# Optimization experiments

Measured on AMD Instinct MI355X. Metric: run time of the kernel, lower is better.

## Reference

```python
import jax, jax.numpy as jnp
import numpy as np

# dims: S slots, B batch, D pred-rep dim, E slot-embedding dim, H hidden/output dim, V per-slot vocab
S, B, D, E, H, V = 7, 4096, 1024, 128, 512, 200
D0 = D + E  # layer-0 LSTM input size


def setup_inputs() -> dict:
    key = jax.random.key(0)
    ks = jax.random.split(key, 12)
    rn = lambda k, shape, s=0.02: jax.random.normal(k, shape, jnp.float32) * s
    return {
        "pred_reps": jax.random.normal(ks[0], (B, D), jnp.float32),
        "slot_labels": jax.random.randint(ks[1], (S, B), 0, V),
        "emb": rn(ks[2], (S, V, E), 1.0),
        # layer 0: per-slot LSTMCell + highway params
        "Wih0": rn(ks[3], (S, 4 * H, D0)), "Whh0": rn(ks[4], (S, 4 * H, H)),
        "bih0": jnp.zeros((S, 4 * H), jnp.float32), "bhh0": jnp.zeros((S, 4 * H), jnp.float32),
        "hwW0": rn(ks[5], (S, H, D0 + H)), "hwb0": jnp.zeros((S, H), jnp.float32),
        "linW0": rn(ks[6], (S, H, D0)),
        # layer 1 (input size = H)
        "Wih1": rn(ks[7], (S, 4 * H, H)), "Whh1": rn(ks[8], (S, 4 * H, H)),
        "bih1": jnp.zeros((S, 4 * H), jnp.float32), "bhh1": jnp.zeros((S, 4 * H), jnp.float32),
        "hwW1": rn(ks[9], (S, H, 2 * H)), "hwb1": jnp.zeros((S, H), jnp.float32),
        "linW1": rn(ks[10], (S, H, H)),
    }


def _lstm_cell(x, h, c, Wih, Whh, bih, bhh):
    # torch LSTMCell: gates ordered i, f, g, o
    gates = x @ Wih.T + bih + h @ Whh.T + bhh
    i, f, g, o = jnp.split(gates, 4, axis=-1)
    c_new = jax.nn.sigmoid(f) * c + jax.nn.sigmoid(i) * jnp.tanh(g)
    h_new = jax.nn.sigmoid(o) * jnp.tanh(c_new)
    return h_new, c_new


def reference(pred_reps, slot_labels, emb, Wih0, Whh0, bih0, bhh0, hwW0, hwb0, linW0,
              Wih1, Whh1, bih1, bhh1, hwW1, hwb1, linW1):
    def step(carry, xs):
        h0, c0, h1, c1 = carry
        (tbl, idx, wih0, whh0, bi0, bh0, hw0, hb0, lw0,
         wih1, whh1, bi1, bh1, hw1, hb1, lw1) = xs
        # per-slot embedding gather + concat with predicate reps  -> [B, D0]
        x = jnp.concatenate([pred_reps, tbl[idx]], axis=-1)
        # layer 0 cell + highway gate
        h0n, c0n = _lstm_cell(x, h0, c0, wih0, whh0, bi0, bh0)
        gate0 = jax.nn.sigmoid(jnp.concatenate([x, h0n], axis=-1) @ hw0.T + hb0)
        x1 = gate0 * h0n + (1.0 - gate0) * (x @ lw0.T)
        # layer 1 cell (its highway output is dead code in the original: curr_input
        # after the last layer is discarded, so we skip it -- same math)
        h1n, c1n = _lstm_cell(x1, h1, c1, wih1, whh1, bi1, bh1)
        return (h0n, c0n, h1n, c1n), None

    init = tuple(jnp.zeros((B, H), pred_reps.dtype) for _ in range(4))
    xs = (emb, slot_labels, Wih0, Whh0, bih0, bhh0, hwW0, hwb0, linW0,
          Wih1, Whh1, bih1, bhh1, hwW1, hwb1, linW1)
    carry, _ = jax.lax.scan(step, init, xs)
    return carry[2]  # last_h: top-layer hidden after final slot
```

## Files before the change

kernel.cpp:

```cpp
#include <hip/hip_runtime.h>
#include <stdint.h>

typedef unsigned short u16;

#define S_   7
#define B_   4096
#define D_   1024
#define E_   128
#define H_   512
#define V_   200
#define D0_  1152
#define XLD  1536
#define K0_  1664
#define KX1  1024
#define G4H  2048

typedef __bf16 bf16x8 __attribute__((ext_vector_type(8)));
typedef float  f32x4  __attribute__((ext_vector_type(4)));
typedef u16    u16x8  __attribute__((ext_vector_type(8)));

__device__ __forceinline__ u16 f2bf(float f) {
  union { float f; uint32_t u; } v; v.f = f;
  uint32_t r = v.u + 0x7fffu + ((v.u >> 16) & 1u);
  return (u16)(r >> 16);
}
__device__ __forceinline__ float bf2f(u16 b) {
  union { uint32_t u; float f; } v; v.u = ((uint32_t)b) << 16;
  return v.f;
}
__device__ __forceinline__ float sigmoidf_(float x) { return 1.0f / (1.0f + __expf(-x)); }
__device__ __forceinline__ float tanhf_(float x) {
  float t = __expf(-2.f * fabsf(x));
  return copysignf((1.f - t) / (1.f + t), x);
}

__device__ __forceinline__ void glds16(const u16* g, u16* l) {
  __builtin_amdgcn_global_load_lds(
      (const __attribute__((address_space(1))) uint32_t*)g,
      (__attribute__((address_space(3))) uint32_t*)l, 16, 0, 0);
}

__device__ __forceinline__ void cvt8(const float* src, u16x8* dst) {
  const float4* p = (const float4*)src;
  float4 x = p[0], y = p[1];
  u16x8 o;
  o[0]=f2bf(x.x); o[1]=f2bf(x.y); o[2]=f2bf(x.z); o[3]=f2bf(x.w);
  o[4]=f2bf(y.x); o[5]=f2bf(y.y); o[6]=f2bf(y.z); o[7]=f2bf(y.w);
  *dst = o;
}

template<int KK, int P1, int P2, int KA, int KB>
__global__ void pack_gw(const float* __restrict__ Wih, const float* __restrict__ Whh,
                        u16* __restrict__ dst) {
  const int CH = KK / 32;
  int i = blockIdx.x * 256 + threadIdx.x;
  int sr = i / CH, c = i - sr * CH;
  int k = c * 32;
  long s = sr >> 11;
  int  r = sr & 2047;
  int  g = r >> 9, j = r & 511;
  long drow = (s << 11) + ((j >> 4) * 64 + g * 16 + (j & 15));
  const float* src = (k < P1) ? Wih + (long)sr * KA + k
                   : (k < P2) ? Whh + (long)sr * KB + (k - P1)
                              : Wih + (long)sr * KA + P1 + (k - P2);
  u16* d = dst + drow * KK + k;
  #pragma unroll
  for (int q = 0; q < 4; ++q) {
    u16x8 o; cvt8(src + q * 8, &o);
    *(u16x8*)(d + q * 8) = o;
  }
}

template<int KS, bool Z2>
__global__ void pack_hw(const float* __restrict__ src, u16* __restrict__ dst, int off16) {
  const int CH = K0_ / 32;
  int i = blockIdx.x * 256 + threadIdx.x;
  int sj = i / CH, c = i - sj * CH;
  int k = c * 32;
  long s = sj >> 9;
  int  j = sj & 511;
  long drow = (s << 10) + ((j >> 4) * 32 + off16 + (j & 15));
  u16* d = dst + drow * K0_ + k;
  if (k >= 1024 && k < 1536 && Z2) {
    u16x8 z = {};
    #pragma unroll
    for (int q = 0; q < 4; ++q) *(u16x8*)(d + q * 8) = z;
    return;
  }
  const float* sp = (k < 1024) ? src + (long)sj * KS + k
                  : (k < 1536) ? src + (long)sj * KS + 1152 + (k - 1024)
                               : src + (long)sj * KS + 1024 + (k - 1536);
  #pragma unroll
  for (int q = 0; q < 4; ++q) {
    u16x8 o; cvt8(sp + q * 8, &o);
    *(u16x8*)(d + q * 8) = o;
  }
}

__global__ void pack_predz(const float* __restrict__ pred, u16* __restrict__ dst) {
  const int CH = XLD / 32;
  int i = blockIdx.x * 256 + threadIdx.x;
  int row = i / CH, c = i - row * CH;
  int k = c * 32;
  u16* d = dst + (long)row * XLD + k;
  if (k < 1024) {
    const float* sp = pred + (long)row * D_ + k;
    #pragma unroll
    for (int q = 0; q < 4; ++q) {
      u16x8 o; cvt8(sp + q * 8, &o);
      *(u16x8*)(d + q * 8) = o;
    }
  } else {
    u16x8 z = {};
    #pragma unroll
    for (int q = 0; q < 4; ++q) *(u16x8*)(d + q * 8) = z;
  }
}

__global__ void xgather(const float* __restrict__ emb, const int* __restrict__ labels,
                        u16* __restrict__ EMB) {
  int b = blockIdx.x;
  int e = threadIdx.x;
  #pragma unroll
  for (int s = 0; s < S_; ++s) {
    int ix = labels[s * B_ + b];
    EMB[((long)(s * B_ + b)) * E_ + e] = f2bf(emb[((long)(s * V_ + ix)) * E_ + e]);
  }
}

__global__ void bias_sum(const float* __restrict__ a, const float* __restrict__ b,
                         float* __restrict__ o, int n) {
  int i = blockIdx.x * 256 + threadIdx.x;
  if (i < n) o[i] = a[i] + b[i];
}
__global__ void zero_f(float* __restrict__ p, int n) {
  for (int i = blockIdx.x * 256 + threadIdx.x; i < n; i += gridDim.x * 256) p[i] = 0.f;
}
__global__ void zero_u16k(u16* __restrict__ p, int n) {
  for (int i = blockIdx.x * 256 + threadIdx.x; i < n; i += gridDim.x * 256) p[i] = 0;
}

template<int MODE>
__global__ __launch_bounds__(256)
void gemm_fused(const u16* __restrict__ A, int lda,
                const u16* __restrict__ EMBs,
                const u16* __restrict__ W, int ldw,
                int K, int TS, int ntn, int cpx,
                const float* __restrict__ bsum,
                float* __restrict__ cbuf,
                u16* __restrict__ hdst, int hld, int hoff,
                float* __restrict__ hf32,
                const u16* __restrict__ xcat0) {
  __shared__ __align__(16) u16 lds[4 * 8192];
  u16* lA = lds;
  u16* lW = lds + 2 * 8192;
  const int tid  = threadIdx.x;
  const int lane = tid & 63;
  const int wave = tid >> 6;
  const int p    = blockIdx.x;
  const int bid  = (p & 7) * cpx + (p >> 3);
  const int tn = bid % ntn;
  const int tm = bid / ntn;
  const long row0 = (long)tm * 128;
  const long col0 = (long)tn * 128;
  const int wm = (wave >> 1) * 64;
  const int wn = (wave & 1) * 64;
  const int fr = lane & 15;
  const int fk = (lane >> 4) * 8;
  const int wr = wave * 32;

  const int srow = wr + (lane >> 3);
  const int scol = ((lane & 7) ^ ((lane >> 3) & 7)) * 8;
  const u16* ga = A + (row0 + srow) * (long)lda + scol;
  const u16* ge = EMBs ? (EMBs + (row0 + srow) * (long)E_ + scol) : nullptr;
  const u16* gw = W + (col0 + srow) * (long)ldw + scol;
  const int dst0 = wr * 64 + lane * 8;

  auto stage = [&](int t, int b) {
    const u16* gb; long ld;
    if (t < TS) { gb = ga + ((long)t << 6);        ld = lda; }
    else        { gb = ge + ((long)(t - TS) << 6); ld = E_;  }
    const u16* gww = gw + ((long)t << 6);
    u16* dA = lA + b * 8192 + dst0;
    u16* dW = lW + b * 8192 + dst0;
    #pragma unroll
    for (int i = 0; i < 4; ++i) {
      glds16(gb  + (long)(i * 8) * ld,  dA + i * 512);
      glds16(gww + (long)(i * 8) * ldw, dW + i * 512);
    }
  };

  int aoff[4], woff[4];
  #pragma unroll
  for (int m = 0; m < 4; ++m) aoff[m] = (wm + m * 16 + fr) * 64;
  #pragma unroll
  for (int n = 0; n < 4; ++n) woff[n] = (wn + n * 16 + fr) * 64;
  const int swz = (fr & 7) << 3;
  const int kk0 = (0 + fk) ^ swz;
  const int kk1 = (32 + fk) ^ swz;

  f32x4 acc[4][4] = {};
  const int nt = K >> 6;

  stage(0, 0);

  for (int t = 0; t < nt; ++t) {
    __syncthreads();
    if (t + 1 < nt) stage(t + 1, (t + 1) & 1);
    const u16* Ab = lA + (t & 1) * 8192;
    const u16* Wb = lW + (t & 1) * 8192;
    bf16x8 af0[4], wf0[4], af1[4], wf1[4];
    #pragma unroll
    for (int m = 0; m < 4; ++m) af0[m] = *(const bf16x8*)&Ab[aoff[m] + kk0];
    #pragma unroll
    for (int n = 0; n < 4; ++n) wf0[n] = *(const bf16x8*)&Wb[woff[n] + kk0];
    #pragma unroll
    for (int m = 0; m < 4; ++m) af1[m] = *(const bf16x8*)&Ab[aoff[m] + kk1];
    #pragma unroll
    for (int n = 0; n < 4; ++n) wf1[n] = *(const bf16x8*)&Wb[woff[n] + kk1];
    #pragma unroll
    for (int m = 0; m < 4; ++m)
      #pragma unroll
      for (int n = 0; n < 4; ++n)
        acc[m][n] = __builtin_amdgcn_mfma_f32_16x16x32_bf16(af0[m], wf0[n], acc[m][n], 0, 0, 0);
    #pragma unroll
    for (int m = 0; m < 4; ++m)
      #pragma unroll
      for (int n = 0; n < 4; ++n)
        acc[m][n] = __builtin_amdgcn_mfma_f32_16x16x32_bf16(af1[m], wf1[n], acc[m][n], 0, 0, 0);
  }

  const int cr = (lane >> 4) * 4;
  const int jg = wn >> 6;

  if (MODE == 0) {
    const int j = tn * 32 + jg * 16 + fr;
    const float bi = bsum[j], bf = bsum[512 + j], bg = bsum[1024 + j], bo = bsum[1536 + j];
    #pragma unroll
    for (int m = 0; m < 4; ++m) {
      const long rbase = row0 + wm + m * 16 + cr;
      #pragma unroll
      for (int r = 0; r < 4; ++r) {
        const long ri = rbase + r;
        float gi = acc[m][0][r] + bi;
        float gf = acc[m][1][r] + bf;
        float gg = acc[m][2][r] + bg;
        float go = acc[m][3][r] + bo;
        float cv = cbuf[ri * H_ + j];
        float cn = sigmoidf_(gf) * cv + sigmoidf_(gi) * tanhf_(gg);
        float hn = sigmoidf_(go) * tanhf_(cn);
        cbuf[ri * H_ + j] = cn;
        hdst[ri * hld + hoff + j] = f2bf(hn);
        if (hf32) hf32[ri * H_ + j] = hn;
      }
    }
  } else {
    #pragma unroll
    for (int pp = 0; pp < 2; ++pp) {
      const int j = tn * 64 + jg * 32 + pp * 16 + fr;
      const float bj = bsum[j];
      #pragma unroll
      for (int m = 0; m < 4; ++m) {
        const long rbase = row0 + wm + m * 16 + cr;
        #pragma unroll
        for (int r = 0; r < 4; ++r) {
          const long ri = rbase + r;
          float gv = sigmoidf_(acc[m][2 * pp][r] + bj);
          float h0 = bf2f(xcat0[ri * XLD + 1024 + j]);
          float x1 = gv * h0 + (1.f - gv) * acc[m][2 * pp + 1][r];
          hdst[ri * hld + hoff + j] = f2bf(x1);
        }
      }
    }
  }
}

extern "C" void kernel_launch(void* const* d_in, const int* in_sizes, int n_in,
                              void* d_out, int out_size, void* d_ws, size_t ws_size,
                              hipStream_t stream) {
  const float* pred   = (const float*)d_in[0];
  const int*   labels = (const int*)d_in[1];
  const float* emb    = (const float*)d_in[2];
  const float* Wih0   = (const float*)d_in[3];
  const float* Whh0   = (const float*)d_in[4];
  const float* bih0   = (const float*)d_in[5];
  const float* bhh0   = (const float*)d_in[6];
  const float* hwW0   = (const float*)d_in[7];
  const float* hwb0   = (const float*)d_in[8];
  const float* linW0  = (const float*)d_in[9];
  const float* Wih1   = (const float*)d_in[10];
  const float* Whh1   = (const float*)d_in[11];
  const float* bih1   = (const float*)d_in[12];
  const float* bhh1   = (const float*)d_in[13];
  float* out = (float*)d_out;

  char* ws = (char*)d_ws;
  size_t off = 0;
  auto alloc = [&](size_t bytes) {
    char* p = ws + off;
    off = (off + bytes + 255) & ~(size_t)255;
    return p;
  };
  u16* WC0   = (u16*)alloc((size_t)S_ * G4H * K0_ * 2);
  u16* WHL   = (u16*)alloc((size_t)S_ * 1024 * K0_ * 2);
  u16* WC1   = (u16*)alloc((size_t)S_ * G4H * KX1 * 2);
  u16* xcat  = (u16*)alloc((size_t)B_ * XLD * 2);
  u16* EMB   = (u16*)alloc((size_t)S_ * B_ * E_ * 2);
  u16* x1cat = (u16*)alloc((size_t)B_ * KX1 * 2);
  float* c0   = (float*)alloc((size_t)B_ * H_ * 4);
  float* c1   = (float*)alloc((size_t)B_ * H_ * 4);
  float* bs0  = (float*)alloc((size_t)S_ * G4H * 4);
  float* bs1  = (float*)alloc((size_t)S_ * G4H * 4);

  pack_gw<K0_, 1024, 1536, D0_, H_><<<2912, 256, 0, stream>>>(Wih0, Whh0, WC0);
  pack_gw<KX1,  512, 1024, H_,  H_><<<1792, 256, 0, stream>>>(Wih1, Whh1, WC1);
  pack_hw<K0_, false><<<728, 256, 0, stream>>>(hwW0,  WHL, 0);
  pack_hw<D0_, true ><<<728, 256, 0, stream>>>(linW0, WHL, 16);
  pack_predz<<<768, 256, 0, stream>>>(pred, xcat);
  xgather<<<B_, E_, 0, stream>>>(emb, labels, EMB);
  bias_sum<<<(S_ * G4H + 255) / 256, 256, 0, stream>>>(bih0, bhh0, bs0, S_ * G4H);
  bias_sum<<<(S_ * G4H + 255) / 256, 256, 0, stream>>>(bih1, bhh1, bs1, S_ * G4H);
  zero_f<<<256, 256, 0, stream>>>(c0, B_ * H_);
  zero_f<<<256, 256, 0, stream>>>(c1, B_ * H_);
  zero_u16k<<<256, 256, 0, stream>>>(x1cat, B_ * KX1);

  const int g0 = (B_ / 128) * (G4H / 128);
  const int g1 = (B_ / 128) * (1024 / 128);

  for (int s = 0; s < S_; ++s) {
    const u16* EMBs = EMB + (size_t)s * B_ * E_;

    gemm_fused<0><<<g0, 256, 0, stream>>>(
        xcat, XLD, EMBs, WC0 + (size_t)s * G4H * K0_, K0_, K0_, 24, G4H / 128, g0 / 8,
        bs0 + (size_t)s * G4H, c0, xcat, XLD, 1024, nullptr, nullptr);

    gemm_fused<1><<<g1, 256, 0, stream>>>(
        xcat, XLD, EMBs, WHL + (size_t)s * 1024 * K0_, K0_, K0_, 24, 1024 / 128, g1 / 8,
        hwb0 + (size_t)s * H_, nullptr, x1cat, KX1, 0, nullptr, xcat);

    gemm_fused<0><<<g0, 256, 0, stream>>>(
        x1cat, KX1, nullptr, WC1 + (size_t)s * G4H * KX1, KX1, KX1, 16, G4H / 128, g0 / 8,
        bs1 + (size_t)s * G4H, c1, x1cat, KX1, H_, out, nullptr);
  }
}
```

Baseline: 699.5 us.

## Wavefront-pipeline the three per-slot GEMMs into one multi-GEMM launch per step

Replaces the 21 sequential per-slot GEMM launches with 9 launches of a combined kernel. Each launch runs layer-0 gates for slot k, the highway step for slot k-1 and layer-1 gates for slot k-2 side by side, using double-buffered (ping-pong) h columns in wider xcat/x1cat buffers to avoid read/write hazards. The goal is fewer launch and tail bubbles and larger grids that keep all CUs busy, at the cost of runtime-dispatched parameters and more workspace. The pack kernels are also rewritten so each thread converts four strided 8-element chunks.

```diff
diff --git a/kernel.cpp b/kernel.cpp
--- a/kernel.cpp
+++ b/kernel.cpp
@@ -10,10 +10,11 @@
 #define H_   512
 #define V_   200
 #define D0_  1152
-#define XLD  1536
 #define K0_  1664
 #define KX1  1024
 #define G4H  2048
+#define XW   2048
+#define X1W  2048
 
 typedef __bf16 bf16x8 __attribute__((ext_vector_type(8)));
 typedef float  f32x4  __attribute__((ext_vector_type(4)));
@@ -40,80 +41,79 @@
       (__attribute__((address_space(3))) uint32_t*)l, 16, 0, 0);
 }
 
-__device__ __forceinline__ void cvt8(const float* src, u16x8* dst) {
+__device__ __forceinline__ void cvt8s(const float* src, u16* dst) {
   const float4* p = (const float4*)src;
   float4 x = p[0], y = p[1];
   u16x8 o;
   o[0]=f2bf(x.x); o[1]=f2bf(x.y); o[2]=f2bf(x.z); o[3]=f2bf(x.w);
   o[4]=f2bf(y.x); o[5]=f2bf(y.y); o[6]=f2bf(y.z); o[7]=f2bf(y.w);
-  *dst = o;
+  *(u16x8*)dst = o;
 }
 
 template<int KK, int P1, int P2, int KA, int KB>
-__global__ void pack_gw(const float* __restrict__ Wih, const float* __restrict__ Whh,
-                        u16* __restrict__ dst) {
-  const int CH = KK / 32;
-  int i = blockIdx.x * 256 + threadIdx.x;
-  int sr = i / CH, c = i - sr * CH;
-  int k = c * 32;
-  long s = sr >> 11;
-  int  r = sr & 2047;
-  int  g = r >> 9, j = r & 511;
-  long drow = (s << 11) + ((j >> 4) * 64 + g * 16 + (j & 15));
-  const float* src = (k < P1) ? Wih + (long)sr * KA + k
-                   : (k < P2) ? Whh + (long)sr * KB + (k - P1)
-                              : Wih + (long)sr * KA + P1 + (k - P2);
-  u16* d = dst + drow * KK + k;
-  #pragma unroll
-  for (int q = 0; q < 4; ++q) {
-    u16x8 o; cvt8(src + q * 8, &o);
-    *(u16x8*)(d + q * 8) = o;
+__global__ void pack_gw4(const float* __restrict__ Wih, const float* __restrict__ Whh,
+                         u16* __restrict__ dst) {
+  const int NG = KK / 8;
+  const int stride = gridDim.x * 256;
+  int idx = blockIdx.x * 256 + threadIdx.x;
+  #pragma unroll
+  for (int u = 0; u < 4; ++u) {
+    int i = idx + u * stride;
+    int sr = i / NG, kg = i - sr * NG;
+    int k8 = kg * 8;
+    long s = sr >> 11;
+    int  r = sr & 2047;
+    int  g = r >> 9, j = r & 511;
+    long drow = (s << 11) + ((j >> 4) * 64 + g * 16 + (j & 15));
+    const float* sp = (k8 < P1) ? Wih + (long)sr * KA + k8
+                    : (k8 < P2) ? Whh + (long)sr * KB + (k8 - P1)
+                                : Wih + (long)sr * KA + P1 + (k8 - P2);
+    cvt8s(sp, &dst[drow * KK + k8]);
   }
 }
 
 template<int KS, bool Z2>
-__global__ void pack_hw(const float* __restrict__ src, u16* __restrict__ dst, int off16) {
-  const int CH = K0_ / 32;
-  int i = blockIdx.x * 256 + threadIdx.x;
-  int sj = i / CH, c = i - sj * CH;
-  int k = c * 32;
-  long s = sj >> 9;
-  int  j = sj & 511;
-  long drow = (s << 10) + ((j >> 4) * 32 + off16 + (j & 15));
-  u16* d = dst + drow * K0_ + k;
-  if (k >= 1024 && k < 1536 && Z2) {
-    u16x8 z = {};
-    #pragma unroll
-    for (int q = 0; q < 4; ++q) *(u16x8*)(d + q * 8) = z;
-    return;
-  }
-  const float* sp = (k < 1024) ? src + (long)sj * KS + k
-                  : (k < 1536) ? src + (long)sj * KS + 1152 + (k - 1024)
-                               : src + (long)sj * KS + 1024 + (k - 1536);
-  #pragma unroll
-  for (int q = 0; q < 4; ++q) {
-    u16x8 o; cvt8(sp + q * 8, &o);
-    *(u16x8*)(d + q * 8) = o;
-  }
-}
-
-__global__ void pack_predz(const float* __restrict__ pred, u16* __restrict__ dst) {
-  const int CH = XLD / 32;
-  int i = blockIdx.x * 256 + threadIdx.x;
-  int row = i / CH, c = i - row * CH;
-  int k = c * 32;
-  u16* d = dst + (long)row * XLD + k;
-  if (k < 1024) {
-    const float* sp = pred + (long)row * D_ + k;
-    #pragma unroll
-    for (int q = 0; q < 4; ++q) {
-      u16x8 o; cvt8(sp + q * 8, &o);
-      *(u16x8*)(d + q * 8) = o;
-    }
-  } else {
-    u16x8 z = {};
-    #pragma unroll
-    for (int q = 0; q < 4; ++q) *(u16x8*)(d + q * 8) = z;
+__global__ void pack_hw4(const float* __restrict__ src, u16* __restrict__ dst, int off16) {
+  const int NG = K0_ / 8;
+  const int stride = gridDim.x * 256;
+  int idx = blockIdx.x * 256 + threadIdx.x;
+  #pragma unroll
+  for (int u = 0; u < 4; ++u) {
+    int i = idx + u * stride;
+    int sj = i / NG, kg = i - sj * NG;
+    int k8 = kg * 8;
+    long s = sj >> 9;
+    int  j = sj & 511;
+    long drow = (s << 10) + ((j >> 4) * 32 + off16 + (j & 15));
+    u16* d = &dst[drow * K0_ + k8];
+    if (Z2 && k8 >= 1024 && k8 < 1536) {
+      u16x8 z = {};
+      *(u16x8*)d = z;
+    } else {
+      const float* sp = (k8 < 1024) ? src + (long)sj * KS + k8
+                      : (k8 < 1536) ? src + (long)sj * KS + 1152 + (k8 - 1024)
+                                    : src + (long)sj * KS + 1024 + (k8 - 1536);
+      cvt8s(sp, d);
+    }
+  }
+}
+
+__global__ void pack_predz4(const float* __restrict__ pred, u16* __restrict__ dst) {
+  const int NG = XW / 8;
+  const int stride = gridDim.x * 256;
+  int idx = blockIdx.x * 256 + threadIdx.x;
+  #pragma unroll
+  for (int u = 0; u < 4; ++u) {
+    int i = idx + u * stride;
+    int row = i / NG, kg = i - row * NG;
+    int k8 = kg * 8;
+    u16* d = &dst[(long)row * XW + k8];
+    if (k8 < 1024) {
+      cvt8s(pred + (long)row * D_ + k8, d);
+    } else {
+      u16x8 z = {};
+      *(u16x8*)d = z;
+    }
   }
 }
 
@@ -140,27 +140,34 @@
   for (int i = blockIdx.x * 256 + threadIdx.x; i < n; i += gridDim.x * 256) p[i] = 0;
 }
 
-template<int MODE>
+struct GemmP {
+  const u16* r0; const u16* r1; const u16* r2;
+  const u16* W;
+  const float* bsum;
+  float* cbuf;
+  u16* hdst;
+  float* hf32;
+  const u16* h0src;
+  int ld0, ld1, ld2, t1, t2, ldw, nt, ntn, cpx, hld, hoff, h0ld, mode;
+};
+
 __global__ __launch_bounds__(256)
-void gemm_fused(const u16* __restrict__ A, int lda,
-                const u16* __restrict__ EMBs,
-                const u16* __restrict__ W, int ldw,
-                int K, int TS, int ntn, int cpx,
-                const float* __restrict__ bsum,
-                float* __restrict__ cbuf,
-                u16* __restrict__ hdst, int hld, int hoff,
-                float* __restrict__ hf32,
-                const u16* __restrict__ xcat0) {
+void gemm_multi(GemmP pa, GemmP pb, GemmP pc, int nA, int nAB) {
   __shared__ __align__(16) u16 lds[4 * 8192];
+  const int b = blockIdx.x;
+  GemmP P = pc; int base = nAB;
+  if (b < nAB) { P = pb; base = nA; }
+  if (b < nA)  { P = pa; base = 0; }
+  const int bidx = b - base;
+
   u16* lA = lds;
   u16* lW = lds + 2 * 8192;
   const int tid  = threadIdx.x;
   const int lane = tid & 63;
   const int wave = tid >> 6;
-  const int p    = blockIdx.x;
-  const int bid  = (p & 7) * cpx + (p >> 3);
-  const int tn = bid % ntn;
-  const int tm = bid / ntn;
+  const int bid  = (bidx & 7) * P.cpx + (bidx >> 3);
+  const int tn = bid % P.ntn;
+  const int tm = bid / P.ntn;
   const long row0 = (long)tm * 128;
   const long col0 = (long)tn * 128;
   const int wm = (wave >> 1) * 64;
@@ -171,22 +178,24 @@
 
   const int srow = wr + (lane >> 3);
   const int scol = ((lane & 7) ^ ((lane >> 3) & 7)) * 8;
-  const u16* ga = A + (row0 + srow) * (long)lda + scol;
-  const u16* ge = EMBs ? (EMBs + (row0 + srow) * (long)E_ + scol) : nullptr;
-  const u16* gw = W + (col0 + srow) * (long)ldw + scol;
+  const u16* gr0 = P.r0 + (row0 + srow) * (long)P.ld0 + scol;
+  const u16* gr1 = P.r1 + (row0 + srow) * (long)P.ld1 + scol;
+  const u16* gr2 = P.r2 + (row0 + srow) * (long)P.ld2 + scol;
+  const u16* gw  = P.W  + (col0 + srow) * (long)P.ldw + scol;
   const int dst0 = wr * 64 + lane * 8;
 
-  auto stage = [&](int t, int b) {
-    const u16* gb; long ld;
-    if (t < TS) { gb = ga + ((long)t << 6);        ld = lda; }
-    else        { gb = ge + ((long)(t - TS) << 6); ld = E_;  }
-    const u16* gww = gw + ((long)t << 6);
-    u16* dA = lA + b * 8192 + dst0;
-    u16* dW = lW + b * 8192 + dst0;
+  auto stage = [&](int t, int buf) {
+    const u16* g; long ld;
+    if (t < P.t1)      { g = gr0 + (long)t * 64;            ld = P.ld0; }
+    else if (t < P.t2) { g = gr1 + (long)(t - P.t1) * 64;   ld = P.ld1; }
+    else               { g = gr2 + (long)(t - P.t2) * 64;   ld = P.ld2; }
+    const u16* gww = gw + (long)t * 64;
+    u16* dA = lA + buf * 8192 + dst0;
+    u16* dW = lW + buf * 8192 + dst0;
     #pragma unroll
     for (int i = 0; i < 4; ++i) {
-      glds16(gb  + (long)(i * 8) * ld,  dA + i * 512);
-      glds16(gww + (long)(i * 8) * ldw, dW + i * 512);
+      glds16(g   + (long)(i * 8) * ld,    dA + i * 512);
+      glds16(gww + (long)(i * 8) * P.ldw, dW + i * 512);
     }
   };
 
@@ -200,7 +209,7 @@
   const int kk1 = (32 + fk) ^ swz;
 
   f32x4 acc[4][4] = {};
-  const int nt = K >> 6;
+  const int nt = P.nt;
 
   stage(0, 0);
 
@@ -233,9 +242,10 @@
   const int cr = (lane >> 4) * 4;
   const int jg = wn >> 6;
 
-  if (MODE == 0) {
+  if (P.mode == 0) {
     const int j = tn * 32 + jg * 16 + fr;
-    const float bi = bsum[j], bf = bsum[512 + j], bg = bsum[1024 + j], bo = bsum[1536 + j];
+    const float bi = P.bsum[j], bf = P.bsum[512 + j];
+    const float bg = P.bsum[1024 + j], bo = P.bsum[1536 + j];
     #pragma unroll
     for (int m = 0; m < 4; ++m) {
       const long rbase = row0 + wm + m * 16 + cr;
@@ -246,19 +256,19 @@
         float gf = acc[m][1][r] + bf;
         float gg = acc[m][2][r] + bg;
         float go = acc[m][3][r] + bo;
-        float cv = cbuf[ri * H_ + j];
+        float cv = P.cbuf[ri * H_ + j];
         float cn = sigmoidf_(gf) * cv + sigmoidf_(gi) * tanhf_(gg);
         float hn = sigmoidf_(go) * tanhf_(cn);
-        cbuf[ri * H_ + j] = cn;
-        hdst[ri * hld + hoff + j] = f2bf(hn);
-        if (hf32) hf32[ri * H_ + j] = hn;
+        P.cbuf[ri * H_ + j] = cn;
+        P.hdst[ri * P.hld + P.hoff + j] = f2bf(hn);
+        if (P.hf32) P.hf32[ri * H_ + j] = hn;
       }
     }
   } else {
     #pragma unroll
     for (int pp = 0; pp < 2; ++pp) {
       const int j = tn * 64 + jg * 32 + pp * 16 + fr;
-      const float bj = bsum[j];
+      const float bj = P.bsum[j];
       #pragma unroll
       for (int m = 0; m < 4; ++m) {
         const long rbase = row0 + wm + m * 16 + cr;
@@ -266,9 +276,9 @@
         for (int r = 0; r < 4; ++r) {
           const long ri = rbase + r;
           float gv = sigmoidf_(acc[m][2 * pp][r] + bj);
-          float h0 = bf2f(xcat0[ri * XLD + 1024 + j]);
+          float h0 = bf2f(P.h0src[ri * (long)P.h0ld + j]);
           float x1 = gv * h0 + (1.f - gv) * acc[m][2 * pp + 1][r];
-          hdst[ri * hld + hoff + j] = f2bf(x1);
+          P.hdst[ri * P.hld + P.hoff + j] = f2bf(x1);
         }
       }
     }
@@ -302,44 +312,78 @@
     return p;
   };
   u16* WC0   = (u16*)alloc((size_t)S_ * G4H * K0_ * 2);
-  u16* WHL   = (u16*)alloc((size_t)S_ * 1024 * K0_ * 2);
+  u16* WHLw  = (u16*)alloc((size_t)S_ * 1024 * K0_ * 2);
   u16* WC1   = (u16*)alloc((size_t)S_ * G4H * KX1 * 2);
-  u16* xcat  = (u16*)alloc((size_t)B_ * XLD * 2);
+  u16* xcat  = (u16*)alloc((size_t)B_ * XW * 2);
   u16* EMB   = (u16*)alloc((size_t)S_ * B_ * E_ * 2);
-  u16* x1cat = (u16*)alloc((size_t)B_ * KX1 * 2);
+  u16* x1cat = (u16*)alloc((size_t)B_ * X1W * 2);
   float* c0   = (float*)alloc((size_t)B_ * H_ * 4);
   float* c1   = (float*)alloc((size_t)B_ * H_ * 4);
   float* bs0  = (float*)alloc((size_t)S_ * G4H * 4);
   float* bs1  = (float*)alloc((size_t)S_ * G4H * 4);
 
-  pack_gw<K0_, 1024, 1536, D0_, H_><<<2912, 256, 0, stream>>>(Wih0, Whh0, WC0);
-  pack_gw<KX1,  512, 1024, H_,  H_><<<1792, 256, 0, stream>>>(Wih1, Whh1, WC1);
-  pack_hw<K0_, false><<<728, 256, 0, stream>>>(hwW0,  WHL, 0);
-  pack_hw<D0_, true ><<<728, 256, 0, stream>>>(linW0, WHL, 16);
-  pack_predz<<<768, 256, 0, stream>>>(pred, xcat);
+  pack_gw4<K0_, 1024, 1536, D0_, H_><<<2912, 256, 0, stream>>>(Wih0, Whh0, WC0);
+  pack_gw4<KX1,  512, 1024, H_,  H_><<<1792, 256, 0, stream>>>(Wih1, Whh1, WC1);
+  pack_hw4<K0_, false><<<728, 256, 0, stream>>>(hwW0,  WHLw, 0);
+  pack_hw4<D0_, true ><<<728, 256, 0, stream>>>(linW0, WHLw, 16);
+  pack_predz4<<<1024, 256, 0, stream>>>(pred, xcat);
   xgather<<<B_, E_, 0, stream>>>(emb, labels, EMB);
-  bias_sum<<<(S_ * G4H + 255) / 256, 256, 0, stream>>>(bih0, bhh0, bs0, S_ * G4H);
-  bias_sum<<<(S_ * G4H + 255) / 256, 256, 0, stream>>>(bih1, bhh1, bs1, S_ * G4H);
+  bias_sum<<<56, 256, 0, stream>>>(bih0, bhh0, bs0, S_ * G4H);
+  bias_sum<<<56, 256, 0, stream>>>(bih1, bhh1, bs1, S_ * G4H);
   zero_f<<<256, 256, 0, stream>>>(c0, B_ * H_);
   zero_f<<<256, 256, 0, stream>>>(c1, B_ * H_);
-  zero_u16k<<<256, 256, 0, stream>>>(x1cat, B_ * KX1);
-
-  const int g0 = (B_ / 128) * (G4H / 128);
-  const int g1 = (B_ / 128) * (1024 / 128);
-
-  for (int s = 0; s < S_; ++s) {
-    const u16* EMBs = EMB + (size_t)s * B_ * E_;
-
-    gemm_fused<0><<<g0, 256, 0, stream>>>(
-        xcat, XLD, EMBs, WC0 + (size_t)s * G4H * K0_, K0_, K0_, 24, G4H / 128, g0 / 8,
-        bs0 + (size_t)s * G4H, c0, xcat, XLD, 1024, nullptr, nullptr);
-
-    gemm_fused<1><<<g1, 256, 0, stream>>>(
-        xcat, XLD, EMBs, WHL + (size_t)s * 1024 * K0_, K0_, K0_, 24, 1024 / 128, g1 / 8,
-        hwb0 + (size_t)s * H_, nullptr, x1cat, KX1, 0, nullptr, xcat);
-
-    gemm_fused<0><<<g0, 256, 0, stream>>>(
-        x1cat, KX1, nullptr, WC1 + (size_t)s * G4H * KX1, KX1, KX1, 16, G4H / 128, g0 / 8,
-        bs1 + (size_t)s * G4H, c1, x1cat, KX1, H_, out, nullptr);
-  }
-}
+  zero_u16k<<<512, 256, 0, stream>>>(x1cat, B_ * X1W);
+
+  auto mkA = [&](int s) {
+    GemmP P;
+    P.r0 = xcat;                                 P.ld0 = XW;  P.t1 = 16;
+    P.r1 = xcat + 1024 + ((s + 1) & 1) * 512;    P.ld1 = XW;  P.t2 = 24;
+    P.r2 = EMB + (size_t)s * B_ * E_;            P.ld2 = E_;
+    P.W = WC0 + (size_t)s * G4H * K0_;           P.ldw = K0_; P.nt = 26;
+    P.ntn = 16; P.cpx = 64;
+    P.bsum = bs0 + (size_t)s * G4H; P.cbuf = c0;
+    P.hdst = xcat; P.hld = XW; P.hoff = 1024 + (s & 1) * 512;
+    P.hf32 = nullptr; P.h0src = xcat; P.h0ld = 0; P.mode = 0;
+    return P;
+  };
+  auto mkB = [&](int s) {
+    GemmP P;
+    P.r0 = xcat;                                 P.ld0 = XW;  P.t1 = 16;
+    P.r1 = xcat + 1024 + (s & 1) * 512;          P.ld1 = XW;  P.t2 = 24;
+    P.r2 = EMB + (size_t)s * B_ * E_;            P.ld2 = E_;
+    P.W = WHLw + (size_t)s * 1024 * K0_;         P.ldw = K0_; P.nt = 26;
+    P.ntn = 8; P.cpx = 32;
+    P.bsum = hwb0 + (size_t)s * H_; P.cbuf = nullptr;
+    P.hdst = x1cat; P.hld = X1W; P.hoff = (s & 1) * 512;
+    P.hf32 = nullptr;
+    P.h0src = xcat + 1024 + (s & 1) * 512; P.h0ld = XW; P.mode = 1;
+    return P;
+  };
+  auto mkC = [&](int s) {
+    GemmP P;
+    P.r0 = x1cat + (s & 1) * 512;                P.ld0 = X1W; P.t1 = 8;
+    P.r1 = x1cat + 1024 + ((s + 1) & 1) * 512;   P.ld1 = X1W; P.t2 = 16;
+    P.r2 = P.r0;                                 P.ld2 = X1W;
+    P.W = WC1 + (size_t)s * G4H * KX1;           P.ldw = KX1; P.nt = 16;
+    P.ntn = 16; P.cpx = 64;
+    P.bsum = bs1 + (size_t)s * G4H; P.cbuf = c1;
+    P.hdst = x1cat; P.hld = X1W; P.hoff = 1024 + (s & 1) * 512;
+    P.hf32 = (s == 6) ? out : nullptr; P.h0src = x1cat; P.h0ld = 0; P.mode = 0;
+    return P;
+  };
+
+  for (int k = 0; k <= 8; ++k) {
+    const int nA = (k <= 6) ? 512 : 0;
+    const int nB = (k >= 1 && k <= 7) ? 256 : 0;
+    const int nC = (k >= 2) ? 512 : 0;
+    GemmP pa, pb, pc;
+    if (nA) pa = mkA(k);
+    if (nB) pb = mkB(k - 1);
+    if (nC) pc = mkC(k - 2);
+    GemmP any = nA ? pa : (nB ? pb : pc);
+    if (!nA) pa = any;
+    if (!nB) pb = any;
+    if (!nC) pc = any;
+    gemm_multi<<<nA + nB + nC, 256, 0, stream>>>(pa, pb, pc, nA, nA + nB);
+  }
+}
```

Result: faster. 660.0 us (-5.6%).
